# Performance work log

Measured on AMD Instinct MI355X. Metric: run time of the kernel, lower is better.

The kernel has to match this reference:

```python
import math
import jax, jax.numpy as jnp
import numpy as np

B, C, H, W = 16, 512, 32, 32
NUM_HEADS = 4
GROUPS = 32
EPS = 1e-5


def setup_inputs() -> dict:
    key = jax.random.key(0)
    ks = jax.random.split(key, 3)
    x = jax.random.normal(ks[0], (B, C, H, W), dtype=jnp.float32)
    # conv weights: kaiming-ish scale for 1x1 convs (fan_in = C)
    qkv_w = jax.random.normal(ks[1], (3 * C, C), dtype=jnp.float32) * (1.0 / math.sqrt(C))
    proj_w = jax.random.normal(ks[2], (C, C), dtype=jnp.float32) * (1.0 / math.sqrt(C))
    return {
        "x": x,
        "norm_w": jnp.ones((C,), jnp.float32),
        "norm_b": jnp.zeros((C,), jnp.float32),
        "qkv_w": qkv_w,
        "qkv_b": jnp.zeros((3 * C,), jnp.float32),
        "proj_w": proj_w,
        "proj_b": jnp.zeros((C,), jnp.float32),
    }


def group_norm(x, w, b):
    bN, c, h, wd = x.shape
    xg = x.reshape(bN, GROUPS, c // GROUPS, h, wd)
    mean = xg.mean(axis=(2, 3, 4), keepdims=True)
    var = xg.var(axis=(2, 3, 4), keepdims=True)
    xg = (xg - mean) * jax.lax.rsqrt(var + EPS)
    x = xg.reshape(bN, c, h, wd)
    return x * w[None, :, None, None] + b[None, :, None, None]


def conv1x1(x, w, b):
    # x: (b,c,h,w), w: (out,in), b: (out,)
    return jnp.einsum('bchw,oc->bohw', x, w) + b[None, :, None, None]


def reference(x, norm_w, norm_b, qkv_w, qkv_b, proj_w, proj_b):
    b, c, h, w = x.shape
    hd = c // NUM_HEADS  # head dim
    n = h * w            # tokens
    qkv = conv1x1(group_norm(x, norm_w, norm_b), qkv_w, qkv_b)
    q, k, v = jnp.split(qkv, 3, axis=1)
    # (b, heads, hd, n)
    q = q.reshape(b, NUM_HEADS, hd, n)
    k = k.reshape(b, NUM_HEADS, hd, n)
    v = v.reshape(b, NUM_HEADS, hd, n)
    # attn: (b, heads, n, n)
    attn = jnp.einsum('bhdn,bhdm->bhnm', q, k) / math.sqrt(hd)
    attn = jax.nn.softmax(attn, axis=-1)
    # out: (b, heads, n, hd) -> (b, c, h, w)
    out = jnp.einsum('bhnm,bhdm->bhnd', attn, v)
    out = out.transpose(0, 1, 3, 2).reshape(b, c, h, w)
    return x + conv1x1(out, proj_w, proj_b)
```

## Files before the change

### kernel.cpp

```cpp
#include <hip/hip_runtime.h>
#include <stdint.h>

#define DEV __device__ __forceinline__

typedef __attribute__((ext_vector_type(4))) float f32x4;
typedef __attribute__((ext_vector_type(8))) short s16x8;
typedef __attribute__((ext_vector_type(8))) __bf16 bf16x8;

constexpr int kB = 16, kC = 512, kN = 1024;
constexpr int kO = 1536;
constexpr int kG = 32, kCPG = 16;
constexpr float kEps = 1e-5f;
constexpr float kQS = 0.08838834764831845f * 1.44269504088896f;

#if __has_builtin(__builtin_amdgcn_exp2f)
#define EXP2(x) __builtin_amdgcn_exp2f(x)
#else
#define EXP2(x) exp2f(x)
#endif

DEV unsigned short f2bf(float f) {
  union { float f; uint32_t u; } cv; cv.f = f;
  uint32_t u = cv.u;
  return (unsigned short)((u + 0x7FFFu + ((u >> 16) & 1u)) >> 16);
}

DEV unsigned short bfbits(float f) {
  __bf16 h = (__bf16)f;
  return __builtin_bit_cast(unsigned short, h);
}

DEV bf16x8 asbf(s16x8 v) { return __builtin_bit_cast(bf16x8, v); }

DEV void gl_lds16(const void* g, void* l) {
  __builtin_amdgcn_global_load_lds(
      (const __attribute__((address_space(1))) uint32_t*)g,
      (__attribute__((address_space(3))) uint32_t*)l, 16, 0, 0);
}

__global__ __launch_bounds__(256) void k_wconv(const float* __restrict__ src,
                                               unsigned short* __restrict__ dst, int n4) {
  int i = blockIdx.x * 256 + threadIdx.x;
  if (i >= n4) return;
  f32x4 v = ((const f32x4*)src)[i];
  unsigned short o[4];
  o[0] = f2bf(v[0]); o[1] = f2bf(v[1]); o[2] = f2bf(v[2]); o[3] = f2bf(v[3]);
  ((uint2*)dst)[i] = *(uint2*)o;
}

__global__ __launch_bounds__(256) void k_gnstats(const float* __restrict__ x,
                                                 float* __restrict__ meanp,
                                                 float* __restrict__ rstdp) {
  int bg = blockIdx.x;
  const f32x4* p4 = (const f32x4*)(x + (size_t)bg * (kCPG * kN));
  float s = 0.f, s2 = 0.f;
  for (int i = threadIdx.x; i < (kCPG * kN / 4); i += 256) {
    f32x4 v = p4[i];
    s += v[0] + v[1] + v[2] + v[3];
    s2 += v[0] * v[0] + v[1] * v[1] + v[2] * v[2] + v[3] * v[3];
  }
#pragma unroll
  for (int m = 32; m >= 1; m >>= 1) { s += __shfl_xor(s, m); s2 += __shfl_xor(s2, m); }
  __shared__ float rb[8];
  int lane = threadIdx.x & 63, wid = threadIdx.x >> 6;
  if (lane == 0) { rb[wid * 2] = s; rb[wid * 2 + 1] = s2; }
  __syncthreads();
  if (threadIdx.x == 0) {
    float S = rb[0] + rb[2] + rb[4] + rb[6];
    float S2 = rb[1] + rb[3] + rb[5] + rb[7];
    float mu = S * (1.f / 16384.f);
    float var = S2 * (1.f / 16384.f) - mu * mu;
    meanp[bg] = mu;
    rstdp[bg] = rsqrtf(var + kEps);
  }
}

__global__ __launch_bounds__(256) void k_gnapply(const float* __restrict__ x,
                                                 const float* __restrict__ gw,
                                                 const float* __restrict__ gb,
                                                 const float* __restrict__ meanp,
                                                 const float* __restrict__ rstdp,
                                                 unsigned short* __restrict__ xt) {
  int bid = blockIdx.x;
  int b = bid >> 7;
  int ct = (bid >> 4) & 7;
  int nt = bid & 15;
  int c0 = ct * 64, n0 = nt * 64;
  __shared__ float tile[64][65];
  int t = threadIdx.x;
#pragma unroll
  for (int pass = 0; pass < 4; ++pass) {
    int r = pass * 16 + (t >> 4);
    int col = (t & 15) << 2;
    int c = c0 + r;
    f32x4 v = *(const f32x4*)(x + ((size_t)b * kC + c) * kN + n0 + col);
    int g = b * kG + (c >> 4);
    float rs = rstdp[g];
    float a = rs * gw[c];
    float bb = gb[c] - meanp[g] * a;
    tile[r][col + 0] = v[0] * a + bb;
    tile[r][col + 1] = v[1] * a + bb;
    tile[r][col + 2] = v[2] * a + bb;
    tile[r][col + 3] = v[3] * a + bb;
  }
  __syncthreads();
#pragma unroll
  for (int pass = 0; pass < 2; ++pass) {
    int nr = pass * 32 + (t >> 3);
    int cb = (t & 7) << 3;
    unsigned short o[8];
#pragma unroll
    for (int j = 0; j < 8; ++j) o[j] = f2bf(tile[cb + j][nr]);
    *(uint4*)(xt + ((size_t)b * kN + n0 + nr) * kC + c0 + cb) = *(uint4*)o;
  }
}

template <int MODE>
__global__ __launch_bounds__(256) void k_gemm(const unsigned short* __restrict__ act,
                                              const unsigned short* __restrict__ wb,
                                              const float* __restrict__ bias,
                                              unsigned short* __restrict__ qkT,
                                              unsigned short* __restrict__ vbuf,
                                              const float* __restrict__ xres,
                                              float* __restrict__ outp) {
  int b = blockIdx.y;
  int nt = blockIdx.x & 7, ot = blockIdx.x >> 3;
  int n0 = nt << 7, o0 = ot << 7;
  int t = threadIdx.x, lane = t & 63, wid = t >> 6;
  int wr = wid >> 1, wc = wid & 1;
  __shared__ unsigned short sA[128 * 64];
  __shared__ unsigned short sB[128 * 64];
  f32x4 acc[4][4];
  const f32x4 zf = {0.f, 0.f, 0.f, 0.f};
#pragma unroll
  for (int i = 0; i < 4; ++i)
#pragma unroll
    for (int j = 0; j < 4; ++j) acc[i][j] = zf;
  const size_t rowb = (size_t)b * kN;
#pragma unroll 1
  for (int kt = 0; kt < 8; ++kt) {
    const int k0 = kt << 6;
    __syncthreads();
#pragma unroll
    for (int p = 0; p < 4; ++p) {
      const int id = p * 256 + t;
      const int row = id >> 3, cp = id & 7;
      const int cl = cp ^ (row & 7);
      gl_lds16(act + (rowb + n0 + row) * (size_t)kC + k0 + cl * 8,
               (char*)sA + (p * 256 + wid * 64) * 16);
      gl_lds16(wb + (size_t)(o0 + row) * kC + k0 + cl * 8,
               (char*)sB + (p * 256 + wid * 64) * 16);
    }
    asm volatile("s_waitcnt vmcnt(0)" ::: "memory");
    __syncthreads();
#pragma unroll
    for (int kk = 0; kk < 2; ++kk) {
      s16x8 af[4], bfr[4];
      const int cl = kk * 4 + (lane >> 4);
#pragma unroll
      for (int i = 0; i < 4; ++i) {
        const int rA = wr * 64 + i * 16 + (lane & 15);
        af[i] = *(const s16x8*)((const char*)sA + rA * 128 + ((cl ^ (rA & 7)) << 4));
        const int rB = wc * 64 + i * 16 + (lane & 15);
        bfr[i] = *(const s16x8*)((const char*)sB + rB * 128 + ((cl ^ (rB & 7)) << 4));
      }
#pragma unroll
      for (int i = 0; i < 4; ++i)
#pragma unroll
        for (int j = 0; j < 4; ++j)
          acc[i][j] = __builtin_amdgcn_mfma_f32_16x16x32_bf16(asbf(af[i]), asbf(bfr[j]),
                                                              acc[i][j], 0, 0, 0);
    }
  }
  const int baseN = n0 + wr * 64 + ((lane >> 4) << 2);
#pragma unroll
  for (int j = 0; j < 4; ++j) {
    const int o = o0 + wc * 64 + j * 16 + (lane & 15);
    const float bs = bias[o];
#pragma unroll
    for (int i = 0; i < 4; ++i) {
      const int nb = baseN + i * 16;
      if (MODE == 0) {
        if (o < 1024) {
          const float sc = (o < 512) ? kQS : 1.0f;
#pragma unroll
          for (int r = 0; r < 4; ++r)
            qkT[(rowb + nb + r) * (size_t)kO + o] = f2bf((acc[i][j][r] + bs) * sc);
        } else {
          unsigned short pk[4];
#pragma unroll
          for (int r = 0; r < 4; ++r) pk[r] = f2bf(acc[i][j][r] + bs);
          *(uint2*)(vbuf + ((size_t)b * 512 + (o - 1024)) * kN + nb) = *(uint2*)pk;
        }
      } else {
        const size_t oo = ((size_t)b * kC + o) * kN + nb;
        const f32x4 xv = *(const f32x4*)(xres + oo);
        f32x4 ov;
        ov[0] = acc[i][j][0] + bs + xv[0];
        ov[1] = acc[i][j][1] + bs + xv[1];
        ov[2] = acc[i][j][2] + bs + xv[2];
        ov[3] = acc[i][j][3] + bs + xv[3];
        *(f32x4*)(outp + oo) = ov;
      }
    }
  }
}

__global__ __launch_bounds__(256, 2) void k_attn(const unsigned short* __restrict__ qkT,
                                                 const unsigned short* __restrict__ vbuf,
                                                 unsigned short* __restrict__ aoT) {
  const int bh = blockIdx.x, qt = blockIdx.y;
  const int b = bh >> 2, h = bh & 3;
  const int t = threadIdx.x, lane = t & 63, wid = t >> 6;
  __shared__ unsigned short sK[2][64 * 128];
  __shared__ unsigned short sV[2][128 * 64];
  __shared__ unsigned short sP[128 * 64];
  const int qrow0 = qt * 128 + wid * 32;
  s16x8 qf[2][4];
#pragma unroll
  for (int bi = 0; bi < 2; ++bi)
#pragma unroll
    for (int kk = 0; kk < 4; ++kk)
      qf[bi][kk] = *(const s16x8*)(qkT + ((size_t)b * kN + qrow0 + bi * 16 + (lane & 15)) * kO +
                                   h * 128 + kk * 32 + ((lane >> 4) << 3));
  f32x4 oc[2][8];
  const f32x4 zf = {0.f, 0.f, 0.f, 0.f};
#pragma unroll
  for (int bi = 0; bi < 2; ++bi)
#pragma unroll
    for (int dj = 0; dj < 8; ++dj) oc[bi][dj] = zf;
  float lpart[8];
#pragma unroll
  for (int i = 0; i < 8; ++i) lpart[i] = 0.f;

  auto stage = [&](int buf, int m0) {
#pragma unroll
    for (int p = 0; p < 4; ++p) {
      const int id = p * 256 + t;
      {
        const int row = id >> 4, cp = id & 15, cl = cp ^ (row & 7);
        gl_lds16(qkT + ((size_t)b * kN + m0 + row) * kO + 512 + h * 128 + cl * 8,
                 (char*)sK[buf] + (p * 256 + wid * 64) * 16);
      }
      {
        const int row = id >> 3, cp = id & 7, cl = cp ^ (row & 7);
        gl_lds16(vbuf + ((size_t)b * 512 + h * 128 + row) * kN + m0 + cl * 8,
                 (char*)sV[buf] + (p * 256 + wid * 64) * 16);
      }
    }
  };

  stage(0, 0);
#pragma unroll 1
  for (int mt = 0; mt < 16; ++mt) {
    const int cur = mt & 1;
    asm volatile("s_waitcnt vmcnt(0)" ::: "memory");
    __syncthreads();
    if (mt < 15) stage(cur ^ 1, (mt + 1) * 64);
    f32x4 sacc[2][4];
#pragma unroll
    for (int bi = 0; bi < 2; ++bi)
#pragma unroll
      for (int j = 0; j < 4; ++j) sacc[bi][j] = zf;
    __builtin_amdgcn_s_setprio(1);
#pragma unroll
    for (int kk = 0; kk < 4; ++kk) {
      s16x8 kf[4];
      const int cl = kk * 4 + (lane >> 4);
#pragma unroll
      for (int j = 0; j < 4; ++j) {
        const int rm = j * 16 + (lane & 15);
        kf[j] = *(const s16x8*)((const char*)sK[cur] + rm * 256 + ((cl ^ (rm & 7)) << 4));
      }
#pragma unroll
      for (int bi = 0; bi < 2; ++bi)
#pragma unroll
        for (int j = 0; j < 4; ++j)
          sacc[bi][j] = __builtin_amdgcn_mfma_f32_16x16x32_bf16(asbf(qf[bi][kk]), asbf(kf[j]),
                                                                sacc[bi][j], 0, 0, 0);
    }
    __builtin_amdgcn_s_setprio(0);
#pragma unroll
    for (int bi = 0; bi < 2; ++bi)
#pragma unroll
      for (int r = 0; r < 4; ++r) {
        const int nrow = wid * 32 + bi * 16 + ((lane >> 4) << 2) + r;
        float pvs = 0.f;
#pragma unroll
        for (int j = 0; j < 4; ++j) {
          const float p = EXP2(sacc[bi][j][r]);
          pvs += p;
          const int m = j * 16 + (lane & 15);
          *(unsigned short*)((char*)sP + nrow * 128 + (((m >> 3) ^ (nrow & 7)) << 4) +
                             ((m & 7) << 1)) = bfbits(p);
        }
        lpart[bi * 4 + r] += pvs;
      }
    __builtin_amdgcn_s_setprio(1);
#pragma unroll
    for (int ks = 0; ks < 2; ++ks) {
      s16x8 pf[2], vf[8];
      const int cl = ks * 4 + (lane >> 4);
#pragma unroll
      for (int bi = 0; bi < 2; ++bi) {
        const int rp = wid * 32 + bi * 16 + (lane & 15);
        pf[bi] = *(const s16x8*)((const char*)sP + rp * 128 + ((cl ^ (rp & 7)) << 4));
      }
#pragma unroll
      for (int dj = 0; dj < 8; ++dj) {
        const int rv = dj * 16 + (lane & 15);
        vf[dj] = *(const s16x8*)((const char*)sV[cur] + rv * 128 + ((cl ^ (rv & 7)) << 4));
      }
#pragma unroll
      for (int bi = 0; bi < 2; ++bi)
#pragma unroll
        for (int dj = 0; dj < 8; ++dj)
          oc[bi][dj] = __builtin_amdgcn_mfma_f32_16x16x32_bf16(asbf(pf[bi]), asbf(vf[dj]),
                                                               oc[bi][dj], 0, 0, 0);
    }
    __builtin_amdgcn_s_setprio(0);
  }
#pragma unroll
  for (int bi = 0; bi < 2; ++bi) {
#pragma unroll
    for (int r = 0; r < 4; ++r) {
      float ls = lpart[bi * 4 + r];
#pragma unroll
      for (int st = 1; st <= 8; st <<= 1) ls += __shfl_xor(ls, st);
      const float inv = 1.f / ls;
      const int n = qrow0 + bi * 16 + ((lane >> 4) << 2) + r;
#pragma unroll
      for (int dj = 0; dj < 8; ++dj) {
        const int d = dj * 16 + (lane & 15);
        aoT[((size_t)b * kN + n) * kC + h * 128 + d] = bfbits(oc[bi][dj][r] * inv);
      }
    }
  }
}

extern "C" void kernel_launch(void* const* d_in, const int* in_sizes, int n_in,
                              void* d_out, int out_size, void* d_ws, size_t ws_size,
                              hipStream_t stream) {
  const float* x = (const float*)d_in[0];
  const float* norm_w = (const float*)d_in[1];
  const float* norm_b = (const float*)d_in[2];
  const float* qkv_w = (const float*)d_in[3];
  const float* qkv_b = (const float*)d_in[4];
  const float* proj_w = (const float*)d_in[5];
  const float* proj_b = (const float*)d_in[6];
  float* out = (float*)d_out;
  char* ws = (char*)d_ws;
  const size_t OFF_MEAN = 0;
  const size_t OFF_RSTD = 2048;
  const size_t OFF_WQ = 4096;
  const size_t OFF_WP = OFF_WQ + (size_t)1536 * 512 * 2;
  const size_t OFF_XT = OFF_WP + (size_t)512 * 512 * 2;
  const size_t OFF_QKT = OFF_XT + (size_t)16 * 1024 * 512 * 2;
  const size_t OFF_V = OFF_QKT + (size_t)16 * 1024 * 1536 * 2;
  const size_t NEED = OFF_V + (size_t)16 * 512 * 1024 * 2;
  if (ws_size < NEED) return;
  float* meanp = (float*)(ws + OFF_MEAN);
  float* rstdp = (float*)(ws + OFF_RSTD);
  unsigned short* wq = (unsigned short*)(ws + OFF_WQ);
  unsigned short* wp = (unsigned short*)(ws + OFF_WP);
  unsigned short* xt = (unsigned short*)(ws + OFF_XT);
  unsigned short* qkT = (unsigned short*)(ws + OFF_QKT);
  unsigned short* vb = (unsigned short*)(ws + OFF_V);
  unsigned short* aoT = xt;

  k_wconv<<<768, 256, 0, stream>>>(qkv_w, wq, 1536 * 512 / 4);
  k_wconv<<<256, 256, 0, stream>>>(proj_w, wp, 512 * 512 / 4);
  k_gnstats<<<512, 256, 0, stream>>>(x, meanp, rstdp);
  k_gnapply<<<2048, 256, 0, stream>>>(x, norm_w, norm_b, meanp, rstdp, xt);
  k_gemm<0><<<dim3(96, 16), 256, 0, stream>>>(xt, wq, qkv_b, qkT, vb, nullptr, nullptr);
  k_attn<<<dim3(64, 8), 256, 0, stream>>>(qkT, vb, aoT);
  k_gemm<1><<<dim3(32, 16), 256, 0, stream>>>(aoT, wp, proj_b, nullptr, nullptr, x, out);
}
```

Before: 133.1 us.

## Double-buffer GEMM LDS tiles and merge weight conversion kernels

```diff
diff --git a/kernel.cpp b/kernel.cpp
--- a/kernel.cpp
+++ b/kernel.cpp
@@ -38,14 +38,21 @@
       (__attribute__((address_space(3))) uint32_t*)l, 16, 0, 0);
 }
 
-__global__ __launch_bounds__(256) void k_wconv(const float* __restrict__ src,
-                                               unsigned short* __restrict__ dst, int n4) {
+__global__ __launch_bounds__(256) void k_wconv2(const float* __restrict__ qw,
+                                                const float* __restrict__ pw,
+                                                unsigned short* __restrict__ dq,
+                                                unsigned short* __restrict__ dp) {
+  const int nq = 1536 * 512 / 4, np = 512 * 512 / 4;
   int i = blockIdx.x * 256 + threadIdx.x;
-  if (i >= n4) return;
-  f32x4 v = ((const f32x4*)src)[i];
+  const float* src;
+  unsigned short* dst;
+  int j;
+  if (i < nq) { src = qw; dst = dq; j = i; }
+  else { j = i - nq; if (j >= np) return; src = pw; dst = dp; }
+  f32x4 v = ((const f32x4*)src)[j];
   unsigned short o[4];
   o[0] = f2bf(v[0]); o[1] = f2bf(v[1]); o[2] = f2bf(v[2]); o[3] = f2bf(v[3]);
-  ((uint2*)dst)[i] = *(uint2*)o;
+  ((uint2*)dst)[j] = *(uint2*)o;
 }
 
 __global__ __launch_bounds__(256) void k_gnstats(const float* __restrict__ x,
@@ -116,20 +123,20 @@
 }
 
 template <int MODE>
-__global__ __launch_bounds__(256) void k_gemm(const unsigned short* __restrict__ act,
-                                              const unsigned short* __restrict__ wb,
-                                              const float* __restrict__ bias,
-                                              unsigned short* __restrict__ qkT,
-                                              unsigned short* __restrict__ vbuf,
-                                              const float* __restrict__ xres,
-                                              float* __restrict__ outp) {
+__global__ __launch_bounds__(256, 2) void k_gemm(const unsigned short* __restrict__ act,
+                                                 const unsigned short* __restrict__ wb,
+                                                 const float* __restrict__ bias,
+                                                 unsigned short* __restrict__ qkT,
+                                                 unsigned short* __restrict__ vbuf,
+                                                 const float* __restrict__ xres,
+                                                 float* __restrict__ outp) {
   int b = blockIdx.y;
   int nt = blockIdx.x & 7, ot = blockIdx.x >> 3;
   int n0 = nt << 7, o0 = ot << 7;
   int t = threadIdx.x, lane = t & 63, wid = t >> 6;
   int wr = wid >> 1, wc = wid & 1;
-  __shared__ unsigned short sA[128 * 64];
-  __shared__ unsigned short sB[128 * 64];
+  __shared__ unsigned short sA[2][128 * 64];
+  __shared__ unsigned short sB[2][128 * 64];
   f32x4 acc[4][4];
   const f32x4 zf = {0.f, 0.f, 0.f, 0.f};
 #pragma unroll
@@ -137,22 +144,29 @@
 #pragma unroll
     for (int j = 0; j < 4; ++j) acc[i][j] = zf;
   const size_t rowb = (size_t)b * kN;
-#pragma unroll 1
-  for (int kt = 0; kt < 8; ++kt) {
+
+  auto stage = [&](int buf, int kt) {
     const int k0 = kt << 6;
-    __syncthreads();
 #pragma unroll
     for (int p = 0; p < 4; ++p) {
       const int id = p * 256 + t;
       const int row = id >> 3, cp = id & 7;
       const int cl = cp ^ (row & 7);
       gl_lds16(act + (rowb + n0 + row) * (size_t)kC + k0 + cl * 8,
-               (char*)sA + (p * 256 + wid * 64) * 16);
+               (char*)sA[buf] + (p * 256 + wid * 64) * 16);
       gl_lds16(wb + (size_t)(o0 + row) * kC + k0 + cl * 8,
-               (char*)sB + (p * 256 + wid * 64) * 16);
-    }
+               (char*)sB[buf] + (p * 256 + wid * 64) * 16);
+    }
+  };
+
+  stage(0, 0);
+#pragma unroll 1
+  for (int kt = 0; kt < 8; ++kt) {
+    const int cur = kt & 1;
     asm volatile("s_waitcnt vmcnt(0)" ::: "memory");
     __syncthreads();
+    if (kt < 7) stage(cur ^ 1, kt + 1);
+    __builtin_amdgcn_s_setprio(1);
 #pragma unroll
     for (int kk = 0; kk < 2; ++kk) {
       s16x8 af[4], bfr[4];
@@ -160,9 +174,9 @@
 #pragma unroll
       for (int i = 0; i < 4; ++i) {
         const int rA = wr * 64 + i * 16 + (lane & 15);
-        af[i] = *(const s16x8*)((const char*)sA + rA * 128 + ((cl ^ (rA & 7)) << 4));
+        af[i] = *(const s16x8*)((const char*)sA[cur] + rA * 128 + ((cl ^ (rA & 7)) << 4));
         const int rB = wc * 64 + i * 16 + (lane & 15);
-        bfr[i] = *(const s16x8*)((const char*)sB + rB * 128 + ((cl ^ (rB & 7)) << 4));
+        bfr[i] = *(const s16x8*)((const char*)sB[cur] + rB * 128 + ((cl ^ (rB & 7)) << 4));
       }
 #pragma unroll
       for (int i = 0; i < 4; ++i)
@@ -171,6 +185,7 @@
           acc[i][j] = __builtin_amdgcn_mfma_f32_16x16x32_bf16(asbf(af[i]), asbf(bfr[j]),
                                                               acc[i][j], 0, 0, 0);
     }
+    __builtin_amdgcn_s_setprio(0);
   }
   const int baseN = n0 + wr * 64 + ((lane >> 4) << 2);
 #pragma unroll
@@ -368,8 +383,7 @@
   unsigned short* vb = (unsigned short*)(ws + OFF_V);
   unsigned short* aoT = xt;
 
-  k_wconv<<<768, 256, 0, stream>>>(qkv_w, wq, 1536 * 512 / 4);
-  k_wconv<<<256, 256, 0, stream>>>(proj_w, wp, 512 * 512 / 4);
+  k_wconv2<<<1024, 256, 0, stream>>>(qkv_w, proj_w, wq, wp);
   k_gnstats<<<512, 256, 0, stream>>>(x, meanp, rstdp);
   k_gnapply<<<2048, 256, 0, stream>>>(x, norm_w, norm_b, meanp, rstdp, xt);
   k_gemm<0><<<dim3(96, 16), 256, 0, stream>>>(xt, wq, qkv_b, qkT, vb, nullptr, nullptr);
```

Measured after the change: 129.4 us. 2.7% less time.
